# Optimization experiments

Measured on AMD Instinct MI355X. Metric: run time of the kernel, lower is better.

The kernel has to match this reference:

```python
import jax, jax.numpy as jnp
import numpy as np

N, C, D = 131072, 512, 3


def setup_inputs() -> dict:
    key = jax.random.key(0)
    kx, kmu = jax.random.split(key)
    X = jax.random.normal(kx, (N, D), dtype=jnp.float32)
    mu = jax.random.normal(kmu, (C, D), dtype=jnp.float32)
    w = jnp.zeros((C,), dtype=jnp.float32)
    # sigma as in __init__: r = sqrt(sum of per-dim unbiased variances of mu0)
    r = jnp.sqrt(jnp.var(mu, axis=0, ddof=1).sum())
    sigma = (0.1 * (r / C ** (1.0 / D))).astype(jnp.float32)
    return {"X": X, "mu": mu, "w": w, "sigma": sigma}


def reference(X, mu, w, sigma):
    # One EM step of a uniform-covariance GMM (EM_step_pytorch).
    n, d = X.shape
    # pairwise squared distances [N, C]
    D2_nc = ((X[:, None, :] - mu[None, :, :]) ** 2).sum(-1)
    # log-responsibilities (E-step), softmax over components
    lgamma_nc = jax.nn.log_softmax(w[None, :] - D2_nc / (2.0 * sigma ** 2), axis=1)
    gamma_nc = jnp.exp(lgamma_nc)
    # M-step: centroids (softmax over points, per component)
    mu_new = jax.nn.softmax(lgamma_nc, axis=0).T @ X  # [C, D]
    # M-step: component scores
    h_c = jax.nn.logsumexp(lgamma_nc, axis=0)  # [C]
    w_new = h_c - h_c.mean()
    # M-step: uniform std
    sigma_new = jnp.sqrt((gamma_nc * D2_nc).sum() / (d * n))
    # EM values: expected targets and free energy
    Y = gamma_nc @ mu_new  # [N, D]
    logpi_c = w_new - jax.nn.logsumexp(w_new)
    Cfe = (gamma_nc * (
        ((mu_new ** 2).sum(-1)[None, :] - (Y ** 2).sum(-1)[:, None]) / (2.0 * sigma_new ** 2)
        + d * jnp.log(sigma_new)
        - logpi_c[None, :]
        + lgamma_nc
    )).sum()
    return Y, Cfe
```

## Files before the change

kernel.cpp:

```cpp
#include <hip/hip_runtime.h>
#include <cfloat>
#include <cmath>

#define NPTS 131072
#define NC   512
#define NREP 4

#define PM4_OFF  0
#define PQ4_OFF  2048
#define ST4_OFF  4096
#define MISC_OFF 12288

__device__ __forceinline__ float waveSum(float v) {
#pragma unroll
  for (int off = 32; off > 0; off >>= 1) v += __shfl_down(v, off, 64);
  return v;
}
__device__ __forceinline__ float waveMax(float v) {
#pragma unroll
  for (int off = 32; off > 0; off >>= 1) v = fmaxf(v, __shfl_down(v, off, 64));
  return v;
}

__global__ __launch_bounds__(512) void k_prep(
    const float* __restrict__ mu, const float* __restrict__ w,
    const float* __restrict__ sigma, float4* __restrict__ pm,
    float* __restrict__ ST, float* __restrict__ misc) {
  const int t = threadIdx.x;
  const float sg = sigma[0];
  const float inv2s2 = 1.0f / (2.0f * sg * sg);
  const float m0 = mu[3 * t], m1 = mu[3 * t + 1], m2 = mu[3 * t + 2];
  pm[t] = make_float4(2.0f * inv2s2 * m0, 2.0f * inv2s2 * m1, 2.0f * inv2s2 * m2,
                      w[t] - (m0 * m0 + m1 * m1 + m2 * m2) * inv2s2);
#pragma unroll
  for (int r = 0; r < NREP * 4; ++r) ST[r * 512 + t] = 0.f;
  if (t < 8) misc[t] = 0.f;
}

__global__ __launch_bounds__(512, 8) void k_estep(
    const float* __restrict__ X, const float4* __restrict__ pm,
    float* __restrict__ ST, float* __restrict__ misc,
    float* __restrict__ out) {
  __shared__ float4 s_pt[128];
  __shared__ float2 s_ms[4][128];
  __shared__ float  s_red[8];
  __shared__ float  s_red2[8];

  const int t = threadIdx.x;
  const int p = t & 127;
  const int ch = __builtin_amdgcn_readfirstlane(t >> 7);
  const int n = blockIdx.x * 128 + p;
  const float x0 = X[3 * n], x1 = X[3 * n + 1], x2 = X[3 * n + 2];

  const float4* __restrict__ pmc = pm + ch * 128;
  float ma = -FLT_MAX, mb = -FLT_MAX, mc = -FLT_MAX, md = -FLT_MAX;
#pragma unroll 4
  for (int i = 0; i < 128; i += 4) {
    float4 a = pmc[i], b = pmc[i + 1], c = pmc[i + 2], d = pmc[i + 3];
    ma = fmaxf(ma, fmaf(a.x, x0, fmaf(a.y, x1, fmaf(a.z, x2, a.w))));
    mb = fmaxf(mb, fmaf(b.x, x0, fmaf(b.y, x1, fmaf(b.z, x2, b.w))));
    mc = fmaxf(mc, fmaf(c.x, x0, fmaf(c.y, x1, fmaf(c.z, x2, c.w))));
    md = fmaxf(md, fmaf(d.x, x0, fmaf(d.y, x1, fmaf(d.z, x2, d.w))));
  }
  const float m = fmaxf(fmaxf(ma, mb), fmaxf(mc, md));
  float sa = 0.f, sb = 0.f, sc = 0.f, sd = 0.f;
#pragma unroll 4
  for (int i = 0; i < 128; i += 4) {
    float4 a = pmc[i], b = pmc[i + 1], c = pmc[i + 2], d = pmc[i + 3];
    sa += __expf(fmaf(a.x, x0, fmaf(a.y, x1, fmaf(a.z, x2, a.w))) - m);
    sb += __expf(fmaf(b.x, x0, fmaf(b.y, x1, fmaf(b.z, x2, b.w))) - m);
    sc += __expf(fmaf(c.x, x0, fmaf(c.y, x1, fmaf(c.z, x2, c.w))) - m);
    sd += __expf(fmaf(d.x, x0, fmaf(d.y, x1, fmaf(d.z, x2, d.w))) - m);
  }
  s_ms[ch][p] = make_float2(m, (sa + sb) + (sc + sd));
  __syncthreads();

  if (t < 128) {
    float2 q0 = s_ms[0][t], q1 = s_ms[1][t], q2 = s_ms[2][t], q3 = s_ms[3][t];
    float M = fmaxf(fmaxf(q0.x, q1.x), fmaxf(q2.x, q3.x));
    float SS = q0.y * __expf(q0.x - M) + q1.y * __expf(q1.x - M) +
               q2.y * __expf(q2.x - M) + q3.y * __expf(q3.x - M);
    float z = M + __logf(SS);
    s_pt[t] = make_float4(x0, x1, x2, z);
    out[3 * n] = z;
  }
  __syncthreads();

  const float4 pc = pm[t];
  float Sg = 0.f, Tx = 0.f, Ty = 0.f, Tz = 0.f, La = 0.f;
#pragma unroll 4
  for (int i = 0; i < 128; ++i) {
    float4 pt = s_pt[i];
    float l = fmaf(pc.x, pt.x, fmaf(pc.y, pt.y, fmaf(pc.z, pt.z, pc.w)));
    float d = l - pt.w;
    float g = __expf(d);
    Sg += g;
    Tx = fmaf(g, pt.x, Tx);
    Ty = fmaf(g, pt.y, Ty);
    Tz = fmaf(g, pt.z, Tz);
    La = fmaf(g, d, La);
  }
  float* st = ST + (((blockIdx.x & (NREP - 1)) * 512 + t) << 2);
  atomicAdd(st + 0, Tx);
  atomicAdd(st + 1, Ty);
  atomicAdd(st + 2, Tz);
  atomicAdd(st + 3, Sg);

  float xx = (t < 128) ? (x0 * x0 + x1 * x1 + x2 * x2) : 0.f;
  float rx = waveSum(xx);
  float rl = waveSum(La);
  if ((t & 63) == 0) { s_red[t >> 6] = rx; s_red2[t >> 6] = rl; }
  __syncthreads();
  if (t == 0) {
    float vx = 0.f, vl = 0.f;
#pragma unroll
    for (int i = 0; i < 8; ++i) { vx += s_red[i]; vl += s_red2[i]; }
    atomicAdd(&misc[0], vx);
    atomicAdd(&misc[3], vl);
  }
}

__global__ __launch_bounds__(512) void k_mstep(
    const float* __restrict__ mu, const float4* __restrict__ ST4,
    float4* __restrict__ pq, float* __restrict__ misc,
    float* __restrict__ out) {
  __shared__ float s_red[8];
  __shared__ float s_red2[8];
  __shared__ float s_bc[4];
  const int t = threadIdx.x;

  float Tx = 0.f, Ty = 0.f, Tz = 0.f, S = 0.f;
#pragma unroll
  for (int r = 0; r < NREP; ++r) {
    float4 v = ST4[r * 512 + t];
    Tx += v.x; Ty += v.y; Tz += v.z; S += v.w;
  }
  const float Sc = fmaxf(S, 1e-30f);
  const float h = __logf(Sc);
  const float m0 = Tx / Sc, m1 = Ty / Sc, m2 = Tz / Sc;

  const float o0 = mu[3 * t], o1 = mu[3 * t + 1], o2 = mu[3 * t + 2];
  const float gdp = S * (o0 * o0 + o1 * o1 + o2 * o2)
                    - 2.0f * (o0 * Tx + o1 * Ty + o2 * Tz);

  float hm = waveMax(h);
  if ((t & 63) == 0) s_red[t >> 6] = hm;
  __syncthreads();
  if (t == 0) {
    float v = s_red[0];
    for (int i = 1; i < 8; ++i) v = fmaxf(v, s_red[i]);
    s_bc[0] = v;
  }
  __syncthreads();
  const float hM = s_bc[0];

  float es = waveSum(__expf(h - hM));
  float gs = waveSum(gdp);
  if ((t & 63) == 0) { s_red[t >> 6] = es; s_red2[t >> 6] = gs; }
  __syncthreads();
  if (t == 0) {
    float esum = 0.f, gsum = 0.f;
    for (int i = 0; i < 8; ++i) { esum += s_red[i]; gsum += s_red2[i]; }
    s_bc[1] = hM + __logf(esum);
    const float gd = fmaxf(misc[0] + gsum, 1e-20f);
    const float sn2 = gd * (1.0f / (3.0f * (float)NPTS));
    s_bc[2] = 1.0f / (2.0f * sn2);
    s_bc[3] = 1.5f * __logf(sn2);
  }
  __syncthreads();

  const float inv2s2n = s_bc[2];
  const float logpi = h - s_bc[1];
  const float A = (m0 * m0 + m1 * m1 + m2 * m2) * inv2s2n - logpi;
  pq[t] = make_float4(m0, m1, m2, A);

  float ca = waveSum(S * A);
  if ((t & 63) == 0) s_red[t >> 6] = ca;
  __syncthreads();
  if (t == 0) {
    float v = 0.f;
    for (int i = 0; i < 8; ++i) v += s_red[i];
    out[NPTS * 3] = v + misc[3] + (float)NPTS * s_bc[3];
    misc[1] = inv2s2n;
  }
}

__global__ __launch_bounds__(512, 8) void k_final(
    const float* __restrict__ X, const float4* __restrict__ pm,
    const float4* __restrict__ pq, const float* __restrict__ misc,
    float* __restrict__ out) {
  __shared__ float4 s_y[4][128];
  __shared__ float  s_red[8];

  const int t = threadIdx.x;
  const int p = t & 127;
  const int ch = __builtin_amdgcn_readfirstlane(t >> 7);
  const int n = blockIdx.x * 128 + p;
  const float x0 = X[3 * n], x1 = X[3 * n + 1], x2 = X[3 * n + 2];
  const float z = out[3 * n];
  const float inv2s2n = misc[1];

  const float4* __restrict__ pmc = pm + ch * 128;
  const float4* __restrict__ pqc = pq + ch * 128;
  float y0 = 0.f, y1 = 0.f, y2 = 0.f;
#pragma unroll 4
  for (int i = 0; i < 128; ++i) {
    float4 pp = pmc[i];
    float4 qq = pqc[i];
    float l = fmaf(pp.x, x0, fmaf(pp.y, x1, fmaf(pp.z, x2, pp.w))) - z;
    float g = __expf(l);
    y0 = fmaf(g, qq.x, y0);
    y1 = fmaf(g, qq.y, y1);
    y2 = fmaf(g, qq.z, y2);
  }
  s_y[ch][p] = make_float4(y0, y1, y2, 0.f);
  __syncthreads();

  float cfe = 0.f;
  if (t < 128) {
    float4 a0 = s_y[0][t], a1 = s_y[1][t], a2 = s_y[2][t], a3 = s_y[3][t];
    float Y0 = (a0.x + a1.x) + (a2.x + a3.x);
    float Y1 = (a0.y + a1.y) + (a2.y + a3.y);
    float Y2 = (a0.z + a1.z) + (a2.z + a3.z);
    cfe = -(Y0 * Y0 + Y1 * Y1 + Y2 * Y2) * inv2s2n;
    out[3 * n] = Y0;
    out[3 * n + 1] = Y1;
    out[3 * n + 2] = Y2;
  }
  float r = waveSum(cfe);
  if ((t & 63) == 0) s_red[t >> 6] = r;
  __syncthreads();
  if (t == 0) {
    float v = 0.f;
#pragma unroll
    for (int i = 0; i < 8; ++i) v += s_red[i];
    atomicAdd(&out[NPTS * 3], v);
  }
}

extern "C" void kernel_launch(void* const* d_in, const int* in_sizes, int n_in,
                              void* d_out, int out_size, void* d_ws, size_t ws_size,
                              hipStream_t stream) {
  const float* X = (const float*)d_in[0];
  const float* mu = (const float*)d_in[1];
  const float* w = (const float*)d_in[2];
  const float* sigma = (const float*)d_in[3];
  float* out = (float*)d_out;
  float* ws = (float*)d_ws;

  float4* pm = (float4*)(ws + PM4_OFF);
  float4* pq = (float4*)(ws + PQ4_OFF);
  float* ST = ws + ST4_OFF;
  float* misc = ws + MISC_OFF;

  k_prep<<<1, 512, 0, stream>>>(mu, w, sigma, pm, ST, misc);
  k_estep<<<NPTS / 128, 512, 0, stream>>>(X, pm, ST, misc, out);
  k_mstep<<<1, 512, 0, stream>>>(mu, (const float4*)ST, pq, misc, out);
  k_final<<<NPTS / 128, 512, 0, stream>>>(X, pm, pq, misc, out);
}
```

Before: 143.1 us.

## Fuse prep and M-step into the E-step and final kernels, using exp2

Drops the single-block prep and M-step kernels. Each E-step and final block now builds the component parameters in shared memory itself, and each final block redundantly recomputes the M-step reduction from the accumulated statistics. Workspace zeroing moves to a memset. Scores are prescaled by log2(e) so the inner loops use exp2 instead of exp, saving a multiply per exponential. This removes two serialized tiny-kernel launches and their global parameter round trips, at the cost of redundant per-block M-step work and extra shared memory per block.

After: 151.2 us. +5.7%, slower.

```diff
diff --git a/kernel.cpp b/kernel.cpp
--- a/kernel.cpp
+++ b/kernel.cpp
@@ -5,9 +5,10 @@
 #define NPTS 131072
 #define NC   512
 #define NREP 4
-
-#define PM4_OFF  0
-#define PQ4_OFF  2048
+#define NT   (NPTS / 128)
+#define L2E  1.4426950408889634f
+#define LN2  0.6931471805599453f
+
 #define ST4_OFF  4096
 #define MISC_OFF 12288
 
@@ -22,25 +23,22 @@
   return v;
 }
 
-__global__ __launch_bounds__(512) void k_prep(
+__device__ __forceinline__ float4 packComp(
     const float* __restrict__ mu, const float* __restrict__ w,
-    const float* __restrict__ sigma, float4* __restrict__ pm,
-    float* __restrict__ ST, float* __restrict__ misc) {
-  const int t = threadIdx.x;
+    const float* __restrict__ sigma, int t) {
   const float sg = sigma[0];
-  const float inv2s2 = 1.0f / (2.0f * sg * sg);
+  const float k2 = L2E / (2.0f * sg * sg);
   const float m0 = mu[3 * t], m1 = mu[3 * t + 1], m2 = mu[3 * t + 2];
-  pm[t] = make_float4(2.0f * inv2s2 * m0, 2.0f * inv2s2 * m1, 2.0f * inv2s2 * m2,
-                      w[t] - (m0 * m0 + m1 * m1 + m2 * m2) * inv2s2);
-#pragma unroll
-  for (int r = 0; r < NREP * 4; ++r) ST[r * 512 + t] = 0.f;
-  if (t < 8) misc[t] = 0.f;
+  return make_float4(2.0f * k2 * m0, 2.0f * k2 * m1, 2.0f * k2 * m2,
+                     w[t] * L2E - (m0 * m0 + m1 * m1 + m2 * m2) * k2);
 }
 
 __global__ __launch_bounds__(512, 8) void k_estep(
-    const float* __restrict__ X, const float4* __restrict__ pm,
+    const float* __restrict__ X, const float* __restrict__ mu,
+    const float* __restrict__ w, const float* __restrict__ sigma,
     float* __restrict__ ST, float* __restrict__ misc,
     float* __restrict__ out) {
+  __shared__ float4 s_pm[NC];
   __shared__ float4 s_pt[128];
   __shared__ float2 s_ms[4][128];
   __shared__ float  s_red[8];
@@ -50,9 +48,13 @@
   const int p = t & 127;
   const int ch = __builtin_amdgcn_readfirstlane(t >> 7);
   const int n = blockIdx.x * 128 + p;
+
+  s_pm[t] = packComp(mu, w, sigma, t);
+  if (blockIdx.x == 0 && t == 0) out[(size_t)NPTS * 3] = 0.f;
   const float x0 = X[3 * n], x1 = X[3 * n + 1], x2 = X[3 * n + 2];
-
-  const float4* __restrict__ pmc = pm + ch * 128;
+  __syncthreads();
+
+  const float4* __restrict__ pmc = s_pm + ch * 128;
   float ma = -FLT_MAX, mb = -FLT_MAX, mc = -FLT_MAX, md = -FLT_MAX;
 #pragma unroll 4
   for (int i = 0; i < 128; i += 4) {
@@ -67,10 +69,10 @@
 #pragma unroll 4
   for (int i = 0; i < 128; i += 4) {
     float4 a = pmc[i], b = pmc[i + 1], c = pmc[i + 2], d = pmc[i + 3];
-    sa += __expf(fmaf(a.x, x0, fmaf(a.y, x1, fmaf(a.z, x2, a.w))) - m);
-    sb += __expf(fmaf(b.x, x0, fmaf(b.y, x1, fmaf(b.z, x2, b.w))) - m);
-    sc += __expf(fmaf(c.x, x0, fmaf(c.y, x1, fmaf(c.z, x2, c.w))) - m);
-    sd += __expf(fmaf(d.x, x0, fmaf(d.y, x1, fmaf(d.z, x2, d.w))) - m);
+    sa += exp2f(fmaf(a.x, x0, fmaf(a.y, x1, fmaf(a.z, x2, a.w))) - m);
+    sb += exp2f(fmaf(b.x, x0, fmaf(b.y, x1, fmaf(b.z, x2, b.w))) - m);
+    sc += exp2f(fmaf(c.x, x0, fmaf(c.y, x1, fmaf(c.z, x2, c.w))) - m);
+    sd += exp2f(fmaf(d.x, x0, fmaf(d.y, x1, fmaf(d.z, x2, d.w))) - m);
   }
   s_ms[ch][p] = make_float2(m, (sa + sb) + (sc + sd));
   __syncthreads();
@@ -78,27 +80,27 @@
   if (t < 128) {
     float2 q0 = s_ms[0][t], q1 = s_ms[1][t], q2 = s_ms[2][t], q3 = s_ms[3][t];
     float M = fmaxf(fmaxf(q0.x, q1.x), fmaxf(q2.x, q3.x));
-    float SS = q0.y * __expf(q0.x - M) + q1.y * __expf(q1.x - M) +
-               q2.y * __expf(q2.x - M) + q3.y * __expf(q3.x - M);
-    float z = M + __logf(SS);
-    s_pt[t] = make_float4(x0, x1, x2, z);
-    out[3 * n] = z;
-  }
-  __syncthreads();
-
-  const float4 pc = pm[t];
-  float Sg = 0.f, Tx = 0.f, Ty = 0.f, Tz = 0.f, La = 0.f;
+    float SS = q0.y * exp2f(q0.x - M) + q1.y * exp2f(q1.x - M) +
+               q2.y * exp2f(q2.x - M) + q3.y * exp2f(q3.x - M);
+    float z2 = M + __log2f(SS);
+    s_pt[t] = make_float4(x0, x1, x2, z2);
+    out[3 * n] = z2;
+  }
+  __syncthreads();
+
+  const float4 pc = s_pm[t];
+  float Sg = 0.f, Tx = 0.f, Ty = 0.f, Tz = 0.f, La2 = 0.f;
 #pragma unroll 4
   for (int i = 0; i < 128; ++i) {
     float4 pt = s_pt[i];
     float l = fmaf(pc.x, pt.x, fmaf(pc.y, pt.y, fmaf(pc.z, pt.z, pc.w)));
     float d = l - pt.w;
-    float g = __expf(d);
+    float g = exp2f(d);
     Sg += g;
     Tx = fmaf(g, pt.x, Tx);
     Ty = fmaf(g, pt.y, Ty);
     Tz = fmaf(g, pt.z, Tz);
-    La = fmaf(g, d, La);
+    La2 = fmaf(g, d, La2);
   }
   float* st = ST + (((blockIdx.x & (NREP - 1)) * 512 + t) << 2);
   atomicAdd(st + 0, Tx);
@@ -108,7 +110,7 @@
 
   float xx = (t < 128) ? (x0 * x0 + x1 * x1 + x2 * x2) : 0.f;
   float rx = waveSum(xx);
-  float rl = waveSum(La);
+  float rl = waveSum(La2 * LN2);
   if ((t & 63) == 0) { s_red[t >> 6] = rx; s_red2[t >> 6] = rl; }
   __syncthreads();
   if (t == 0) {
@@ -120,14 +122,26 @@
   }
 }
 
-__global__ __launch_bounds__(512) void k_mstep(
-    const float* __restrict__ mu, const float4* __restrict__ ST4,
-    float4* __restrict__ pq, float* __restrict__ misc,
+__global__ __launch_bounds__(512, 8) void k_final(
+    const float* __restrict__ X, const float* __restrict__ mu,
+    const float* __restrict__ w, const float* __restrict__ sigma,
+    const float4* __restrict__ ST4, const float* __restrict__ misc,
     float* __restrict__ out) {
-  __shared__ float s_red[8];
-  __shared__ float s_red2[8];
-  __shared__ float s_bc[4];
+  __shared__ float4 s_pm[NC];
+  __shared__ float4 s_pq[NC];
+  __shared__ float4 s_y[4][128];
+  __shared__ float  s_red[8];
+  __shared__ float  s_red2[8];
+  __shared__ float  s_bc[4];
+
   const int t = threadIdx.x;
+  const int p = t & 127;
+  const int ch = __builtin_amdgcn_readfirstlane(t >> 7);
+  const int n = blockIdx.x * 128 + p;
+
+  s_pm[t] = packComp(mu, w, sigma, t);
+  const float x0 = X[3 * n], x1 = X[3 * n + 1], x2 = X[3 * n + 2];
+  const float z2 = out[3 * n];
 
   float Tx = 0.f, Ty = 0.f, Tz = 0.f, S = 0.f;
 #pragma unroll
@@ -172,43 +186,27 @@
   const float inv2s2n = s_bc[2];
   const float logpi = h - s_bc[1];
   const float A = (m0 * m0 + m1 * m1 + m2 * m2) * inv2s2n - logpi;
-  pq[t] = make_float4(m0, m1, m2, A);
+  s_pq[t] = make_float4(m0, m1, m2, A);
 
   float ca = waveSum(S * A);
   if ((t & 63) == 0) s_red[t >> 6] = ca;
   __syncthreads();
-  if (t == 0) {
+  if (t == 0 && blockIdx.x == 0) {
     float v = 0.f;
+#pragma unroll
     for (int i = 0; i < 8; ++i) v += s_red[i];
-    out[NPTS * 3] = v + misc[3] + (float)NPTS * s_bc[3];
-    misc[1] = inv2s2n;
-  }
-}
-
-__global__ __launch_bounds__(512, 8) void k_final(
-    const float* __restrict__ X, const float4* __restrict__ pm,
-    const float4* __restrict__ pq, const float* __restrict__ misc,
-    float* __restrict__ out) {
-  __shared__ float4 s_y[4][128];
-  __shared__ float  s_red[8];
-
-  const int t = threadIdx.x;
-  const int p = t & 127;
-  const int ch = __builtin_amdgcn_readfirstlane(t >> 7);
-  const int n = blockIdx.x * 128 + p;
-  const float x0 = X[3 * n], x1 = X[3 * n + 1], x2 = X[3 * n + 2];
-  const float z = out[3 * n];
-  const float inv2s2n = misc[1];
-
-  const float4* __restrict__ pmc = pm + ch * 128;
-  const float4* __restrict__ pqc = pq + ch * 128;
+    atomicAdd(&out[(size_t)NPTS * 3], v + misc[3] + (float)NPTS * s_bc[3]);
+  }
+
+  const float4* __restrict__ pmc = s_pm + ch * 128;
+  const float4* __restrict__ pqc = s_pq + ch * 128;
   float y0 = 0.f, y1 = 0.f, y2 = 0.f;
 #pragma unroll 4
   for (int i = 0; i < 128; ++i) {
     float4 pp = pmc[i];
     float4 qq = pqc[i];
-    float l = fmaf(pp.x, x0, fmaf(pp.y, x1, fmaf(pp.z, x2, pp.w))) - z;
-    float g = __expf(l);
+    const float l = fmaf(pp.x, x0, fmaf(pp.y, x1, fmaf(pp.z, x2, pp.w))) - z2;
+    const float g = exp2f(l);
     y0 = fmaf(g, qq.x, y0);
     y1 = fmaf(g, qq.y, y1);
     y2 = fmaf(g, qq.z, y2);
@@ -219,9 +217,9 @@
   float cfe = 0.f;
   if (t < 128) {
     float4 a0 = s_y[0][t], a1 = s_y[1][t], a2 = s_y[2][t], a3 = s_y[3][t];
-    float Y0 = (a0.x + a1.x) + (a2.x + a3.x);
-    float Y1 = (a0.y + a1.y) + (a2.y + a3.y);
-    float Y2 = (a0.z + a1.z) + (a2.z + a3.z);
+    const float Y0 = (a0.x + a1.x) + (a2.x + a3.x);
+    const float Y1 = (a0.y + a1.y) + (a2.y + a3.y);
+    const float Y2 = (a0.z + a1.z) + (a2.z + a3.z);
     cfe = -(Y0 * Y0 + Y1 * Y1 + Y2 * Y2) * inv2s2n;
     out[3 * n] = Y0;
     out[3 * n + 1] = Y1;
@@ -234,7 +232,7 @@
     float v = 0.f;
 #pragma unroll
     for (int i = 0; i < 8; ++i) v += s_red[i];
-    atomicAdd(&out[NPTS * 3], v);
+    atomicAdd(&out[(size_t)NPTS * 3], v);
   }
 }
 
@@ -248,13 +246,10 @@
   float* out = (float*)d_out;
   float* ws = (float*)d_ws;
 
-  float4* pm = (float4*)(ws + PM4_OFF);
-  float4* pq = (float4*)(ws + PQ4_OFF);
   float* ST = ws + ST4_OFF;
   float* misc = ws + MISC_OFF;
 
-  k_prep<<<1, 512, 0, stream>>>(mu, w, sigma, pm, ST, misc);
-  k_estep<<<NPTS / 128, 512, 0, stream>>>(X, pm, ST, misc, out);
-  k_mstep<<<1, 512, 0, stream>>>(mu, (const float4*)ST, pq, misc, out);
-  k_final<<<NPTS / 128, 512, 0, stream>>>(X, pm, pq, misc, out);
-}
+  hipMemsetAsync(ST, 0, (size_t)(NREP * NC * 4 + 8) * sizeof(float), stream);
+  k_estep<<<NT, 512, 0, stream>>>(X, mu, w, sigma, ST, misc, out);
+  k_final<<<NT, 512, 0, stream>>>(X, mu, w, sigma, (const float4*)ST, misc, out);
+}
```
